# Kernel tuning notes

Measured on AMD Instinct MI355X. Metric: run time of the kernel, lower is better.

The kernel has to match this reference:

```python
import jax, jax.numpy as jnp
import numpy as np

K = 3        # kernel_size
PAD = 1      # padding
STRIDE = 1   # stride (must be 1: module asserts offset HxW == input HxW)
DIL = 1      # dilation


def _bilinear_gather(x, py, px):
    """x: (B,C,H,W); py,px: (B,KK,Ho,Wo) float sample coords.
    Returns (B,C,KK,Ho,Wo), zero outside bounds (DCNv2 semantics)."""
    B, C, H, W = x.shape
    y0 = jnp.floor(py); x0 = jnp.floor(px)
    wy1 = py - y0; wy0 = 1.0 - wy1
    wx1 = px - x0; wx0 = 1.0 - wx1
    flat = x.reshape(B, C, H * W)

    def gather(yi, xi):
        valid = (yi >= 0) & (yi < H) & (xi >= 0) & (xi < W)
        yc = jnp.clip(yi, 0, H - 1).astype(jnp.int32)
        xc = jnp.clip(xi, 0, W - 1).astype(jnp.int32)
        idx = (yc * W + xc).reshape(B, 1, -1)                      # (B,1,KK*Ho*Wo)
        g = jnp.take_along_axis(flat, jnp.broadcast_to(idx, (B, C, idx.shape[-1])), axis=2)
        g = g.reshape(B, C, *yi.shape[1:])                          # (B,C,KK,Ho,Wo)
        return jnp.where(valid[:, None], g, 0.0)

    v00 = gather(y0, x0)
    v01 = gather(y0, x0 + 1)
    v10 = gather(y0 + 1, x0)
    v11 = gather(y0 + 1, x0 + 1)
    wy0 = wy0[:, None]; wy1 = wy1[:, None]; wx0 = wx0[:, None]; wx1 = wx1[:, None]
    return wy0 * (wx0 * v00 + wx1 * v01) + wy1 * (wx0 * v10 + wx1 * v11)


def dcn_v2(x, coord_offset, coord_weight, weight, bias):
    B, C, H, W = x.shape
    O = weight.shape[0]
    KK = K * K
    # offset channels ordered (k, [y,x]) per DCNv2 layout
    offs = coord_offset.reshape(B, KK, 2, H, W)
    oy, ox = offs[:, :, 0], offs[:, :, 1]
    ky, kx = jnp.meshgrid(jnp.arange(K), jnp.arange(K), indexing='ij')
    ky = ky.reshape(KK); kx = kx.reshape(KK)
    # base sampling grid for each output pixel / kernel tap: (KK,H,W)
    py = (jnp.arange(H) * STRIDE - PAD)[None, :, None] + (ky * DIL)[:, None, None]
    px = (jnp.arange(W) * STRIDE - PAD)[None, None, :] + (kx * DIL)[:, None, None]
    py = py.astype(x.dtype)[None] + oy   # (B,KK,H,W)
    px = px.astype(x.dtype)[None] + ox
    sampled = _bilinear_gather(x, py, px)              # (B,C,KK,H,W)
    sampled = sampled * coord_weight[:, None]          # modulation mask
    out = jnp.einsum('bckhw,ock->bohw', sampled, weight.reshape(O, C, KK))
    return out + bias[None, :, None, None]


def setup_inputs() -> dict:
    key = jax.random.key(0)
    k1, k2, k3, k4, k5 = jax.random.split(key, 5)
    B, C, O, H, W = 8, 256, 256, 64, 64
    return {
        'input': jax.random.normal(k1, (B, C, H, W), dtype=jnp.float32),
        'coord_offset': jax.random.normal(k2, (B, 2 * K * K, H, W), dtype=jnp.float32),
        'coord_weight': jax.random.uniform(k3, (B, K * K, H, W), dtype=jnp.float32),
        'weight': jax.random.normal(k4, (O, C, K, K), dtype=jnp.float32) * 0.02,
        'bias': jax.random.normal(k5, (O,), dtype=jnp.float32) * 0.01,
    }


def reference(input, coord_offset, coord_weight, weight, bias):
    return dcn_v2(input, coord_offset, coord_weight, weight, bias)
```

## Files before the change

kernel.cpp:

```cpp
#include <hip/hip_runtime.h>
#include <hip/hip_bf16.h>
#include <stdint.h>

typedef _Float16 f16_t;
typedef f16_t f16x8 __attribute__((ext_vector_type(8)));
typedef float f32x4 __attribute__((ext_vector_type(4)));

__device__ inline void lgkm_barrier() {
    __builtin_amdgcn_s_waitcnt(0xC07F);
    __builtin_amdgcn_s_barrier();
}

__global__ __launch_bounds__(512) void k_prep(const float* __restrict__ x,
                                              const float* __restrict__ w,
                                              f16_t* __restrict__ xt,
                                              f16_t* __restrict__ Wp) {
    __shared__ __align__(16) float lw[9216];
    const int t = threadIdx.x;
    if (blockIdx.x < 512) {
        const int b = blockIdx.x >> 6;
        const int y = blockIdx.x & 63;
        const float* src = x + ((size_t)(b * 256) * 64 + y) * 64;
        const int x4 = (t & 15) * 4;
        const int c0 = (t >> 4) * 8;
        float4 v[8];
#pragma unroll
        for (int e = 0; e < 8; ++e)
            v[e] = *(const float4*)(src + (size_t)(c0 + e) * 4096 + x4);
        f16_t* dst = xt + ((size_t)(b * 64 + y) * 64) * 256;
#pragma unroll
        for (int j = 0; j < 4; ++j) {
            f16x8 o;
#pragma unroll
            for (int e = 0; e < 8; ++e) {
                const float f = (j == 0) ? v[e].x : (j == 1) ? v[e].y
                              : (j == 2) ? v[e].z : v[e].w;
                o[e] = (f16_t)f;
            }
            *(f16x8*)(dst + (x4 + j) * 256 + c0) = o;
        }
    } else {
        const int o0 = (blockIdx.x - 512) * 4;
        const float4* srcw = (const float4*)(w + (size_t)o0 * 2304);
#pragma unroll
        for (int i = 0; i < 5; ++i) {
            const int idx = t + 512 * i;
            if (idx < 2304) ((float4*)lw)[idx] = srcw[idx];
        }
        __syncthreads();
#pragma unroll
        for (int i = 0; i < 3; ++i) {
            const int u = t + 512 * i;
            if (u < 1152) {
                const int o = u / 288, r = u - o * 288;
                const int kb2 = r >> 3, rr = r & 7;
                const int s = rr >> 2, qq = rr & 3;
                const int kk = kb2 >> 2, cp = kb2 & 3;
                f16x8 vv;
#pragma unroll
                for (int e = 0; e < 8; ++e) {
                    const int c = cp * 64 + s * 32 + qq * 8 + e;
                    vv[e] = (f16_t)lw[o * 2304 + c * 9 + kk];
                }
                *(f16x8*)(Wp + (size_t)kb2 * 16384 + s * 8192 + qq * 2048
                              + (size_t)(o0 + o) * 8) = vv;
            }
        }
    }
}

__global__ __launch_bounds__(1024, 4) void k_dcn(
    const f16_t* __restrict__ xt, const f16_t* __restrict__ Wp,
    const float* __restrict__ coff, const float* __restrict__ cwm,
    const float* __restrict__ bias, float* __restrict__ out) {

    __shared__ __align__(16) f16_t sS[2][128 * 64];
    __shared__ __align__(16) f16_t sA[2][16384];
    __shared__ __align__(16) int2 sT[9 * 128 * 4];

    const int blk = blockIdx.x;
    const int b  = blk & 7;
    const int hb = blk >> 3;
    const int h0 = hb * 2;
    const int t = threadIdx.x;
    const int wv = t >> 6;
    const int lane = t & 63;
    const int mg = wv >> 1;
    const int ng = wv & 1;

    const int p = t >> 3;
    const int q = t & 7;

    const int fr = lane & 15;
    const int quad = lane >> 4;
    const int swz = fr & 7;

    for (int u = t; u < 1152; u += 1024) {
        const int kk = u >> 7, pp = u & 127;
        const int hr = pp >> 6, wpx = pp & 63;
        const int h = h0 + hr;
        float oy = coff[((size_t)(b * 18 + kk * 2 + 0) * 64 + h) * 64 + wpx];
        float ox = coff[((size_t)(b * 18 + kk * 2 + 1) * 64 + h) * 64 + wpx];
        float m  = cwm [((size_t)(b * 9 + kk) * 64 + h) * 64 + wpx];
        float py = (float)(h - 1 + (kk / 3)) + oy;
        float px = (float)(wpx - 1 + (kk % 3)) + ox;
        float fy = floorf(py), fx = floorf(px);
        int y0 = (int)fy, x0 = (int)fx;
        int y1 = y0 + 1,  x1 = x0 + 1;
        float wy1 = py - fy, wx1 = px - fx;
        float wy0 = 1.0f - wy1, wx0 = 1.0f - wx1;
        bool vy0 = (y0 >= 0) && (y0 < 64), vy1 = (y1 >= 0) && (y1 < 64);
        bool vx0 = (x0 >= 0) && (x0 < 64), vx1 = (x1 >= 0) && (x1 < 64);
        int yc0 = min(max(y0, 0), 63), yc1 = min(max(y1, 0), 63);
        int xc0 = min(max(x0, 0), 63), xc1 = min(max(x1, 0), 63);
        const int base = b * 4096;
        float cw[4];
        int   ca[4];
        cw[0] = (vy0 && vx0) ? wy0 * wx0 * m : 0.0f;
        cw[1] = (vy0 && vx1) ? wy0 * wx1 * m : 0.0f;
        cw[2] = (vy1 && vx0) ? wy1 * wx0 * m : 0.0f;
        cw[3] = (vy1 && vx1) ? wy1 * wx1 * m : 0.0f;
        ca[0] = (base + yc0 * 64 + xc0) * 512;
        ca[1] = (base + yc0 * 64 + xc1) * 512;
        ca[2] = (base + yc1 * 64 + xc0) * 512;
        ca[3] = (base + yc1 * 64 + xc1) * 512;
#pragma unroll
        for (int c = 0; c < 4; ++c) {
            unsigned short ws = __builtin_bit_cast(unsigned short, (f16_t)cw[c]);
            sT[(kk * 128 + pp) * 4 + c] = make_int2(ca[c], (int)ws);
        }
    }
    __syncthreads();

    f16_t* const swb0 = &sS[0][p * 64 + ((q ^ (p & 7)) * 8)];
    const int qb = q * 16;
    const char* xb = (const char*)xt;

    f32x4 acc[2][4] = {};
    f16x8 g0, g1, g2, g3;
    f16x8 sld0, sld1;
    int4 t0, t1;

    auto stage_load = [&](int it) {
        const f16_t* g = Wp + (size_t)it * 16384 + wv * 1024 + lane * 8;
        sld0 = *(const f16x8*)(g);
        sld1 = *(const f16x8*)(g + 512);
    };
    auto stage_write = [&](int buf) {
        f16_t* l = &sA[buf][wv * 1024 + lane * 8];
        *(f16x8*)(l)       = sld0;
        *(f16x8*)(l + 512) = sld1;
    };

    auto gather_issue = [&](int it) {
        const int kk = it >> 2, cp = it & 3;
        if ((it & 3) == 0) {
            const int4* tp = (const int4*)&sT[(kk * 128 + p) * 4];
            t0 = tp[0];
            t1 = tp[1];
        }
        const int cb = cp * 128 + qb;
        g0 = *(const f16x8*)(xb + (t0.x + cb));
        g1 = *(const f16x8*)(xb + (t0.z + cb));
        g2 = *(const f16x8*)(xb + (t1.x + cb));
        g3 = *(const f16x8*)(xb + (t1.z + cb));
    };

    auto combine_write = [&](int buf) {
        f16_t w0 = __builtin_bit_cast(f16_t, (unsigned short)t0.y);
        f16_t w1 = __builtin_bit_cast(f16_t, (unsigned short)t0.w);
        f16_t w2 = __builtin_bit_cast(f16_t, (unsigned short)t1.y);
        f16_t w3 = __builtin_bit_cast(f16_t, (unsigned short)t1.w);
        f16x8 w0v = {w0, w0, w0, w0, w0, w0, w0, w0};
        f16x8 w1v = {w1, w1, w1, w1, w1, w1, w1, w1};
        f16x8 w2v = {w2, w2, w2, w2, w2, w2, w2, w2};
        f16x8 w3v = {w3, w3, w3, w3, w3, w3, w3, w3};
        f16x8 ov = g0 * w0v + g1 * w1v + g2 * w2v + g3 * w3v;
        *(f16x8*)(swb0 + buf * 8192) = ov;
    };

    auto do_mfma = [&](int cur) {
        const f16_t* sb = &sS[cur][ng * 4096];
        const f16_t* sa = &sA[cur][quad * 2048 + mg * 256 + fr * 8];
        f16x8 aC[2][2];
        aC[0][0] = *(const f16x8*)(sa);
        aC[0][1] = *(const f16x8*)(sa + 8192);
        aC[1][0] = *(const f16x8*)(sa + 128);
        aC[1][1] = *(const f16x8*)(sa + 8192 + 128);
        __builtin_amdgcn_s_setprio(1);
#pragma unroll
        for (int s = 0; s < 2; ++s) {
            const int coffe = ((s * 4 + quad) ^ swz) * 8;
            f16x8 bb[4];
#pragma unroll
            for (int nt = 0; nt < 4; ++nt)
                bb[nt] = *(const f16x8*)(sb + (nt * 16 + fr) * 64 + coffe);
#pragma unroll
            for (int mt = 0; mt < 2; ++mt)
#pragma unroll
                for (int nt = 0; nt < 4; ++nt)
                    acc[mt][nt] = __builtin_amdgcn_mfma_f32_16x16x32_f16(
                        aC[mt][s], bb[nt], acc[mt][nt], 0, 0, 0);
        }
        __builtin_amdgcn_s_setprio(0);
    };

    stage_load(0);
    gather_issue(0);
    combine_write(0);
    stage_write(0);
    lgkm_barrier();

    for (int it2 = 0; it2 < 36; it2 += 2) {
        stage_load(it2 + 1);
        gather_issue(it2 + 1);
        __builtin_amdgcn_sched_barrier(0);
        do_mfma(0);
        __builtin_amdgcn_sched_barrier(0);
        combine_write(1);
        stage_write(1);
        lgkm_barrier();

        const bool more = (it2 + 2) < 36;
        if (more) {
            stage_load(it2 + 2);
            gather_issue(it2 + 2);
        }
        __builtin_amdgcn_sched_barrier(0);
        do_mfma(1);
        __builtin_amdgcn_sched_barrier(0);
        if (more) {
            combine_write(0);
            stage_write(0);
        }
        lgkm_barrier();
    }

    const int rowq = quad * 4;
#pragma unroll
    for (int mt = 0; mt < 2; ++mt) {
#pragma unroll
        for (int r = 0; r < 4; ++r) {
            const int og = mg * 32 + mt * 16 + rowq + r;
            const float bs = bias[og];
            float* opn = out + ((size_t)(b * 256 + og) * 64 + (h0 + ng)) * 64;
#pragma unroll
            for (int nt = 0; nt < 4; ++nt) {
                opn[nt * 16 + fr] = acc[mt][nt][r] + bs;
            }
        }
    }
}

extern "C" void kernel_launch(void* const* d_in, const int* in_sizes, int n_in,
                              void* d_out, int out_size, void* d_ws, size_t ws_size,
                              hipStream_t stream) {
    const float* x    = (const float*)d_in[0];
    const float* coff = (const float*)d_in[1];
    const float* cwm  = (const float*)d_in[2];
    const float* wgt  = (const float*)d_in[3];
    const float* bias = (const float*)d_in[4];
    float* out = (float*)d_out;

    f16_t* xt = (f16_t*)d_ws;
    f16_t* Wp = xt + (size_t)8 * 64 * 64 * 256;

    k_prep<<<576, 512, 0, stream>>>(x, wgt, xt, Wp);
    k_dcn <<<256, 1024, 0, stream>>>(xt, Wp, coff, cwm, bias, out);
}
```

Before: 145.8 us.

## Deepen gather/weight prefetch to two iterations ahead with dual register sets

Global gathers and weight-tile loads are now issued two iterations ahead into alternating even/odd register sets. This gives each load a full extra MFMA phase to arrive before its combine and LDS write. Each set keeps the tap weights extracted at issue time, so the later refresh of the t0/t1 table registers cannot corrupt a combine still waiting to run. The cost is higher VGPR pressure from the doubled staging registers, which could reduce occupancy or cause spills.

```diff
diff --git a/kernel.cpp b/kernel.cpp
--- a/kernel.cpp
+++ b/kernel.cpp
@@ -137,46 +137,45 @@
     const char* xb = (const char*)xt;
 
     f32x4 acc[2][4] = {};
-    f16x8 g0, g1, g2, g3;
-    f16x8 sld0, sld1;
     int4 t0, t1;
-
-    auto stage_load = [&](int it) {
-        const f16_t* g = Wp + (size_t)it * 16384 + wv * 1024 + lane * 8;
-        sld0 = *(const f16x8*)(g);
-        sld1 = *(const f16x8*)(g + 512);
-    };
-    auto stage_write = [&](int buf) {
-        f16_t* l = &sA[buf][wv * 1024 + lane * 8];
-        *(f16x8*)(l)       = sld0;
-        *(f16x8*)(l + 512) = sld1;
-    };
-
-    auto gather_issue = [&](int it) {
+    f16x8 gE[4], gO[4];
+    f16_t wsE[4], wsO[4];
+    f16x8 sldE[2], sldO[2];
+
+    auto issue = [&](int it, f16x8 (&g)[4], f16_t (&wsv)[4], f16x8 (&sld)[2]) {
         const int kk = it >> 2, cp = it & 3;
         if ((it & 3) == 0) {
             const int4* tp = (const int4*)&sT[(kk * 128 + p) * 4];
             t0 = tp[0];
             t1 = tp[1];
         }
+        const f16_t* gp = Wp + (size_t)it * 16384 + wv * 1024 + lane * 8;
+        sld[0] = *(const f16x8*)(gp);
+        sld[1] = *(const f16x8*)(gp + 512);
         const int cb = cp * 128 + qb;
-        g0 = *(const f16x8*)(xb + (t0.x + cb));
-        g1 = *(const f16x8*)(xb + (t0.z + cb));
-        g2 = *(const f16x8*)(xb + (t1.x + cb));
-        g3 = *(const f16x8*)(xb + (t1.z + cb));
-    };
-
-    auto combine_write = [&](int buf) {
-        f16_t w0 = __builtin_bit_cast(f16_t, (unsigned short)t0.y);
-        f16_t w1 = __builtin_bit_cast(f16_t, (unsigned short)t0.w);
-        f16_t w2 = __builtin_bit_cast(f16_t, (unsigned short)t1.y);
-        f16_t w3 = __builtin_bit_cast(f16_t, (unsigned short)t1.w);
-        f16x8 w0v = {w0, w0, w0, w0, w0, w0, w0, w0};
-        f16x8 w1v = {w1, w1, w1, w1, w1, w1, w1, w1};
-        f16x8 w2v = {w2, w2, w2, w2, w2, w2, w2, w2};
-        f16x8 w3v = {w3, w3, w3, w3, w3, w3, w3, w3};
-        f16x8 ov = g0 * w0v + g1 * w1v + g2 * w2v + g3 * w3v;
+        g[0] = *(const f16x8*)(xb + (t0.x + cb));
+        g[1] = *(const f16x8*)(xb + (t0.z + cb));
+        g[2] = *(const f16x8*)(xb + (t1.x + cb));
+        g[3] = *(const f16x8*)(xb + (t1.z + cb));
+        wsv[0] = __builtin_bit_cast(f16_t, (unsigned short)t0.y);
+        wsv[1] = __builtin_bit_cast(f16_t, (unsigned short)t0.w);
+        wsv[2] = __builtin_bit_cast(f16_t, (unsigned short)t1.y);
+        wsv[3] = __builtin_bit_cast(f16_t, (unsigned short)t1.w);
+    };
+
+    auto combine_write = [&](int buf, f16x8 (&g)[4], f16_t (&wsv)[4]) {
+        f16x8 w0v = {wsv[0], wsv[0], wsv[0], wsv[0], wsv[0], wsv[0], wsv[0], wsv[0]};
+        f16x8 w1v = {wsv[1], wsv[1], wsv[1], wsv[1], wsv[1], wsv[1], wsv[1], wsv[1]};
+        f16x8 w2v = {wsv[2], wsv[2], wsv[2], wsv[2], wsv[2], wsv[2], wsv[2], wsv[2]};
+        f16x8 w3v = {wsv[3], wsv[3], wsv[3], wsv[3], wsv[3], wsv[3], wsv[3], wsv[3]};
+        f16x8 ov = g[0] * w0v + g[1] * w1v + g[2] * w2v + g[3] * w3v;
         *(f16x8*)(swb0 + buf * 8192) = ov;
+    };
+
+    auto stage_write = [&](int buf, f16x8 (&sld)[2]) {
+        f16_t* l = &sA[buf][wv * 1024 + lane * 8];
+        *(f16x8*)(l)       = sld[0];
+        *(f16x8*)(l + 512) = sld[1];
     };
 
     auto do_mfma = [&](int cur) {
@@ -205,33 +204,28 @@
         __builtin_amdgcn_s_setprio(0);
     };
 
-    stage_load(0);
-    gather_issue(0);
-    combine_write(0);
-    stage_write(0);
+    issue(0, gE, wsE, sldE);
+    combine_write(0, gE, wsE);
+    stage_write(0, sldE);
+    issue(1, gO, wsO, sldO);
     lgkm_barrier();
 
     for (int it2 = 0; it2 < 36; it2 += 2) {
-        stage_load(it2 + 1);
-        gather_issue(it2 + 1);
+        if (it2 + 2 < 36) issue(it2 + 2, gE, wsE, sldE);
         __builtin_amdgcn_sched_barrier(0);
         do_mfma(0);
         __builtin_amdgcn_sched_barrier(0);
-        combine_write(1);
-        stage_write(1);
+        combine_write(1, gO, wsO);
+        stage_write(1, sldO);
         lgkm_barrier();
 
-        const bool more = (it2 + 2) < 36;
-        if (more) {
-            stage_load(it2 + 2);
-            gather_issue(it2 + 2);
-        }
+        if (it2 + 3 < 36) issue(it2 + 3, gO, wsO, sldO);
         __builtin_amdgcn_sched_barrier(0);
         do_mfma(1);
         __builtin_amdgcn_sched_barrier(0);
-        if (more) {
-            combine_write(0);
-            stage_write(0);
+        if (it2 + 2 < 36) {
+            combine_write(0, gE, wsE);
+            stage_write(0, sldE);
         }
         lgkm_barrier();
     }
```

After: 206.6 us. +41.7%, slower.

## Fuse prep and DCN kernels into one launch with grid-wide atomic barrier

Applied to the files above, without the earlier changes.

Merges the input transpose/f16 conversion and weight repacking into the main DCN kernel. Each of the 256 blocks converts two rows of x and repacks one output channel's weights, computes its sampling table, then waits at a global atomic-counter barrier before the GEMM phase. This removes one kernel launch and the gap between kernels, but it adds a memset launch and relies on all 256 blocks being co-resident. The spin barrier has a timeout budget, so if blocks are not co-resident it can fall through and read data that has not been written yet.

```diff
diff --git a/kernel.cpp b/kernel.cpp
--- a/kernel.cpp
+++ b/kernel.cpp
@@ -11,23 +11,33 @@
     __builtin_amdgcn_s_barrier();
 }
 
-__global__ __launch_bounds__(512) void k_prep(const float* __restrict__ x,
-                                              const float* __restrict__ w,
-                                              f16_t* __restrict__ xt,
-                                              f16_t* __restrict__ Wp) {
-    __shared__ __align__(16) float lw[9216];
+__global__ __launch_bounds__(1024, 4) void k_all(
+    const float* __restrict__ x, const float* __restrict__ w,
+    const float* __restrict__ coff, const float* __restrict__ cwm,
+    const float* __restrict__ bias, float* __restrict__ out,
+    f16_t* __restrict__ xt, f16_t* __restrict__ Wp,
+    unsigned int* __restrict__ ctr) {
+
+    __shared__ __align__(16) f16_t sS[2][128 * 64];
+    __shared__ __align__(16) f16_t sA[2][16384];
+    __shared__ __align__(16) int2 sT[9 * 128 * 4];
+
+    const int blk = blockIdx.x;
     const int t = threadIdx.x;
-    if (blockIdx.x < 512) {
-        const int b = blockIdx.x >> 6;
-        const int y = blockIdx.x & 63;
-        const float* src = x + ((size_t)(b * 256) * 64 + y) * 64;
-        const int x4 = (t & 15) * 4;
-        const int c0 = (t >> 4) * 8;
+
+    {
+        const int task = blk * 2 + (t >> 9);
+        const int u = t & 511;
+        const int tb = task >> 6;
+        const int ty = task & 63;
+        const float* src = x + ((size_t)(tb * 256) * 64 + ty) * 64;
+        const int x4 = (u & 15) * 4;
+        const int c0 = (u >> 4) * 8;
         float4 v[8];
 #pragma unroll
         for (int e = 0; e < 8; ++e)
             v[e] = *(const float4*)(src + (size_t)(c0 + e) * 4096 + x4);
-        f16_t* dst = xt + ((size_t)(b * 64 + y) * 64) * 256;
+        f16_t* dst = xt + ((size_t)(tb * 64 + ty) * 64) * 256;
 #pragma unroll
         for (int j = 0; j < 4; ++j) {
             f16x8 o;
@@ -39,50 +49,25 @@
             }
             *(f16x8*)(dst + (x4 + j) * 256 + c0) = o;
         }
-    } else {
-        const int o0 = (blockIdx.x - 512) * 4;
-        const float4* srcw = (const float4*)(w + (size_t)o0 * 2304);
-#pragma unroll
-        for (int i = 0; i < 5; ++i) {
-            const int idx = t + 512 * i;
-            if (idx < 2304) ((float4*)lw)[idx] = srcw[idx];
-        }
-        __syncthreads();
-#pragma unroll
-        for (int i = 0; i < 3; ++i) {
-            const int u = t + 512 * i;
-            if (u < 1152) {
-                const int o = u / 288, r = u - o * 288;
-                const int kb2 = r >> 3, rr = r & 7;
-                const int s = rr >> 2, qq = rr & 3;
-                const int kk = kb2 >> 2, cp = kb2 & 3;
-                f16x8 vv;
-#pragma unroll
-                for (int e = 0; e < 8; ++e) {
-                    const int c = cp * 64 + s * 32 + qq * 8 + e;
-                    vv[e] = (f16_t)lw[o * 2304 + c * 9 + kk];
-                }
-                *(f16x8*)(Wp + (size_t)kb2 * 16384 + s * 8192 + qq * 2048
-                              + (size_t)(o0 + o) * 8) = vv;
-            }
-        }
-    }
-}
-
-__global__ __launch_bounds__(1024, 4) void k_dcn(
-    const f16_t* __restrict__ xt, const f16_t* __restrict__ Wp,
-    const float* __restrict__ coff, const float* __restrict__ cwm,
-    const float* __restrict__ bias, float* __restrict__ out) {
-
-    __shared__ __align__(16) f16_t sS[2][128 * 64];
-    __shared__ __align__(16) f16_t sA[2][16384];
-    __shared__ __align__(16) int2 sT[9 * 128 * 4];
-
-    const int blk = blockIdx.x;
+    }
+    if (t < 288) {
+        const int o = blk;
+        const int kb2 = t >> 3, rr = t & 7;
+        const int s = rr >> 2, qq = rr & 3;
+        const int kk = kb2 >> 2, cp = kb2 & 3;
+        f16x8 vv;
+#pragma unroll
+        for (int e = 0; e < 8; ++e) {
+            const int c = cp * 64 + s * 32 + qq * 8 + e;
+            vv[e] = (f16_t)w[(size_t)o * 2304 + c * 9 + kk];
+        }
+        *(f16x8*)(Wp + (size_t)kb2 * 16384 + s * 8192 + qq * 2048
+                      + (size_t)o * 8) = vv;
+    }
+
     const int b  = blk & 7;
     const int hb = blk >> 3;
     const int h0 = hb * 2;
-    const int t = threadIdx.x;
     const int wv = t >> 6;
     const int lane = t & 63;
     const int mg = wv >> 1;
@@ -130,6 +115,18 @@
             sT[(kk * 128 + pp) * 4 + c] = make_int2(ca[c], (int)ws);
         }
     }
+
+    __syncthreads();
+    if (t == 0) {
+        __threadfence();
+        __hip_atomic_fetch_add(ctr, 1u, __ATOMIC_ACQ_REL,
+                               __HIP_MEMORY_SCOPE_AGENT);
+        int budget = 1 << 22;
+        while (__hip_atomic_load(ctr, __ATOMIC_ACQUIRE,
+                                 __HIP_MEMORY_SCOPE_AGENT) < 256u && --budget)
+            __builtin_amdgcn_s_sleep(8);
+        __threadfence();
+    }
     __syncthreads();
 
     f16_t* const swb0 = &sS[0][p * 64 + ((q ^ (p & 7)) * 8)];
@@ -264,7 +261,9 @@
 
     f16_t* xt = (f16_t*)d_ws;
     f16_t* Wp = xt + (size_t)8 * 64 * 64 * 256;
-
-    k_prep<<<576, 512, 0, stream>>>(x, wgt, xt, Wp);
-    k_dcn <<<256, 1024, 0, stream>>>(xt, Wp, coff, cwm, bias, out);
+    unsigned int* ctr = (unsigned int*)(Wp + (size_t)36 * 16384);
+
+    hipMemsetAsync(ctr, 0, 4, stream);
+    void* args_unused = nullptr; (void)args_unused;
+    k_all<<<256, 1024, 0, stream>>>(x, wgt, coff, cwm, bias, out, xt, Wp, ctr);
 }
```

New measurement: 181.5 us. 24.5% more time.
